# Kernel tuning notes

Measured on AMD Instinct MI355X. Metric: run time of the kernel, lower is better.

Reference implementation:

```python
import jax, jax.numpy as jnp
import numpy as np

B, T, V = 4, 2048, 2048
D = 256   # state_dim
R = 512   # inner_dim
EPS = float(jnp.finfo(jnp.float32).eps)  # F.rms_norm default eps = dtype eps


def rms_norm(x):
    return x * jax.lax.rsqrt(jnp.mean(x * x, axis=-1, keepdims=True) + EPS)


def setup_inputs() -> dict:
    key = jax.random.key(0)
    ks = jax.random.split(key, 9)
    std = 0.02
    return {
        "x": jax.random.normal(ks[0], (B, T, V), dtype=jnp.float32),
        "Wq": jax.random.normal(ks[1], (D, V), dtype=jnp.float32) * std,
        "Wk": jax.random.normal(ks[2], (D, V), dtype=jnp.float32) * std,
        "Wv": jax.random.normal(ks[3], (D, V), dtype=jnp.float32) * std,
        "Wo": jax.random.normal(ks[4], (V, D), dtype=jnp.float32) * std,
        "decay_logit": jnp.float32(3.0),
        "q_out_scale": jnp.float32(0.1),
        "Wdown": jax.random.normal(ks[5], (R, V), dtype=jnp.float32) * std,
        "Wup": jax.random.normal(ks[6], (V, R), dtype=jnp.float32) * std,
        "t_bias": jnp.zeros((R,), dtype=jnp.float32),
        "t_out_scale": jnp.float32(0.1),
        "q_scale": jnp.ones((1,), dtype=jnp.float32),
        "t_scale": jnp.ones((1,), dtype=jnp.float32),
    }


def qtable(x, Wq, Wk, Wv, Wo, decay_logit, out_scale):
    # x: (B,T,V)
    q = jnp.einsum('btv,dv->btd', x, Wq)
    k = jnp.einsum('btv,dv->btd', x, Wk)
    v = jnp.einsum('btv,dv->btd', x, Wv)
    scores = jnp.einsum('btd,bsd->bts', q, k)  # (B,T,T)
    decay = jax.nn.sigmoid(decay_logit)
    pos = jnp.arange(T)
    diff = pos[None, :] - pos[:, None]  # diff[t,s] = s - t ... matches torch (unsqueeze(0)-unsqueeze(1))
    causal = (diff > 0).astype(jnp.float32)
    weights = decay ** jnp.clip(diff.astype(jnp.float32) - 1.0, 0.0, None) * causal
    scores = scores * weights[None, :, :]
    retrieved = jnp.einsum('bts,bsd->btd', scores, v)
    return jnp.einsum('btd,vd->btv', retrieved, Wo) * out_scale


def transform(x, Wdown, Wup, bias, out_scale):
    h = jnp.einsum('btv,rv->btr', x, Wdown) + bias
    h = jax.nn.gelu(h, approximate=False)
    return jnp.einsum('btr,vr->btv', h, Wup) * out_scale


def reference(x, Wq, Wk, Wv, Wo, decay_logit, q_out_scale,
              Wdown, Wup, t_bias, t_out_scale, q_scale, t_scale):
    x = x + q_scale * qtable(rms_norm(x), Wq, Wk, Wv, Wo, decay_logit, q_out_scale)
    x = x + t_scale * transform(rms_norm(x), Wdown, Wup, t_bias, t_out_scale)
    return x
```

## Files before the change

kernel.cpp:

```cpp
#include <hip/hip_runtime.h>
#include <cmath>

typedef _Float16 f16;
typedef _Float16 f16x8 __attribute__((ext_vector_type(8)));
typedef _Float16 f16x4 __attribute__((ext_vector_type(4)));
typedef float f32x4 __attribute__((ext_vector_type(4)));

#define MFMA16(a, b, c) __builtin_amdgcn_mfma_f32_16x16x32_f16(a, b, c, 0, 0, 0)

static constexpr int Bsz = 4;
static constexpr int T = 2048;
static constexpr int V = 2048;
static constexpr int D = 256;
static constexpr int R = 512;
static constexpr int M = Bsz * T;

__device__ __forceinline__ void load_lds16(const f16* g, f16* l) {
    __builtin_amdgcn_global_load_lds(
        (const __attribute__((address_space(1))) unsigned int*)(unsigned long long)g,
        (__attribute__((address_space(3))) unsigned int*)(unsigned int)(unsigned long long)l,
        16, 0, 0);
}

__global__ __launch_bounds__(256) void conv_all(const float* __restrict__ s0,
                                                const float* __restrict__ s1,
                                                const float* __restrict__ s2,
                                                const float* __restrict__ s3,
                                                const float* __restrict__ s4,
                                                const float* __restrict__ s5,
                                                f16* __restrict__ dst) {
    int idx = (blockIdx.x * 256 + threadIdx.x) * 4;
    if (idx >= 4194304) return;
    const float* src; int off;
    if      (idx <  524288) { src = s0; off = idx; }
    else if (idx < 1048576) { src = s1; off = idx - 524288; }
    else if (idx < 1572864) { src = s2; off = idx - 1048576; }
    else if (idx < 2097152) { src = s3; off = idx - 1572864; }
    else if (idx < 3145728) { src = s4; off = idx - 2097152; }
    else                    { src = s5; off = idx - 3145728; }
    float4 v = *(const float4*)&src[off];
    f16x4 o;
    o[0] = (f16)v.x; o[1] = (f16)v.y; o[2] = (f16)v.z; o[3] = (f16)v.w;
    *(f16x4*)&dst[idx] = o;
}

__global__ __launch_bounds__(256) void rmsnorm_kernel(const float* __restrict__ x,
                                                      f16* __restrict__ out) {
    int row = blockIdx.x;
    const float* xr = x + (size_t)row * V;
    int tid = threadIdx.x;
    float4 v0 = ((const float4*)xr)[tid];
    float4 v1 = ((const float4*)xr)[tid + 256];
    float ss = v0.x * v0.x + v0.y * v0.y + v0.z * v0.z + v0.w * v0.w
             + v1.x * v1.x + v1.y * v1.y + v1.z * v1.z + v1.w * v1.w;
    #pragma unroll
    for (int o = 32; o > 0; o >>= 1) ss += __shfl_xor(ss, o);
    __shared__ float wsum[4];
    if ((tid & 63) == 0) wsum[tid >> 6] = ss;
    __syncthreads();
    float tot = wsum[0] + wsum[1] + wsum[2] + wsum[3];
    float s = rsqrtf(tot / (float)V + 1.1920929e-07f);
    f16* orow = out + (size_t)row * V;
    f16x4 o0, o1;
    o0[0] = (f16)(v0.x * s); o0[1] = (f16)(v0.y * s);
    o0[2] = (f16)(v0.z * s); o0[3] = (f16)(v0.w * s);
    o1[0] = (f16)(v1.x * s); o1[1] = (f16)(v1.y * s);
    o1[2] = (f16)(v1.z * s); o1[3] = (f16)(v1.w * s);
    *(f16x4*)&orow[tid * 4] = o0;
    *(f16x4*)&orow[1024 + tid * 4] = o1;
}

__global__ __launch_bounds__(256) void rmsnorm_f16(const f16* __restrict__ x,
                                                   f16* __restrict__ out) {
    int row = blockIdx.x;
    int tid = threadIdx.x;
    const f16* xr = x + (size_t)row * V;
    f16x8 v = *(const f16x8*)&xr[tid * 8];
    float f[8];
    float ss = 0.f;
    #pragma unroll
    for (int j = 0; j < 8; j++) { f[j] = (float)v[j]; ss += f[j] * f[j]; }
    #pragma unroll
    for (int o = 32; o > 0; o >>= 1) ss += __shfl_xor(ss, o);
    __shared__ float wsum[4];
    if ((tid & 63) == 0) wsum[tid >> 6] = ss;
    __syncthreads();
    float tot = wsum[0] + wsum[1] + wsum[2] + wsum[3];
    float s = rsqrtf(tot / (float)V + 1.1920929e-07f);
    f16x8 o;
    #pragma unroll
    for (int j = 0; j < 8; j++) o[j] = (f16)(f[j] * s);
    *(f16x8*)&out[(size_t)row * V + tid * 8] = o;
}

struct GemmEpi {
    const float* residf;
    const f16* residh;
    float* outf;
    f16* outh;
    f16* out_q; f16* out_k; f16* out_vT;
    f16* out_h;
    const float* bias;
    const float* sA; const float* sB;
};

template <int MODE>
__device__ __forceinline__ void epi_store(const GemmEpi& e, float s, f32x4 a,
                                          int gm_base, int gn) {
    #pragma unroll
    for (int i = 0; i < 4; i++) {
        int gm = gm_base + i;
        float vv = a[i];
        if (MODE == 0) {
            if (gn < 256) {
                e.out_q[(size_t)gm * D + gn] = (f16)vv;
            } else if (gn < 512) {
                e.out_k[(size_t)gm * D + (gn - 256)] = (f16)vv;
            } else {
                int d = gn - 512;
                int b = gm >> 11, t = gm & 2047;
                e.out_vT[((size_t)b * D + d) * T + t] = (f16)vv;
            }
        } else if (MODE == 1) {
            size_t o = (size_t)gm * V + gn;
            e.outh[o] = (f16)(e.residf[o] + s * vv);
        } else if (MODE == 2) {
            float z = vv + e.bias[gn];
            float g = 0.5f * z * (1.f + erff(z * 0.70710678118654752f));
            e.out_h[(size_t)gm * R + gn] = (f16)g;
        } else {
            size_t o = (size_t)gm * V + gn;
            e.outf[o] = (float)e.residh[o] + s * vv;
        }
    }
}

template <int MODE>
__global__ __launch_bounds__(256) void gemm_nt(const f16* __restrict__ A,
                                               const f16* __restrict__ Bm,
                                               int K, GemmEpi e) {
    __shared__ f16 Asl[2][128 * 32];
    __shared__ f16 Bsl[2][128 * 32];
    int tid = threadIdx.x;
    int lane = tid & 63, wv = tid >> 6;
    int wm = wv >> 1, wn = wv & 1;
    int quad = lane >> 4, l16 = lane & 15;
    int m0 = blockIdx.x * 128, n0 = blockIdx.y * 128;
    f32x4 acc[4][4] = {};

    int srow = lane >> 2;
    int scg = (lane & 3) ^ ((lane >> 3) & 3);
    const f16* Ag0 = &A[(size_t)(m0 + 16 * wv + srow) * K + scg * 8];
    const f16* Ag1 = &A[(size_t)(m0 + 16 * (wv + 4) + srow) * K + scg * 8];
    const f16* Bg0 = &Bm[(size_t)(n0 + 16 * wv + srow) * K + scg * 8];
    const f16* Bg1 = &Bm[(size_t)(n0 + 16 * (wv + 4) + srow) * K + scg * 8];
    int lo0 = (16 * wv) * 32, lo1 = (16 * (wv + 4)) * 32;

    int fs = quad ^ ((l16 >> 1) & 3);
    int niter = K >> 5;

    load_lds16(Ag0, &Asl[0][lo0]);
    load_lds16(Ag1, &Asl[0][lo1]);
    load_lds16(Bg0, &Bsl[0][lo0]);
    load_lds16(Bg1, &Bsl[0][lo1]);

    for (int i = 0; i < niter; i++) {
        int cur = i & 1;
        __builtin_amdgcn_s_barrier();
        if (i + 1 < niter) {
            int k0 = (i + 1) << 5;
            int nb = cur ^ 1;
            load_lds16(Ag0 + k0, &Asl[nb][lo0]);
            load_lds16(Ag1 + k0, &Asl[nb][lo1]);
            load_lds16(Bg0 + k0, &Bsl[nb][lo0]);
            load_lds16(Bg1 + k0, &Bsl[nb][lo1]);
            asm volatile("s_waitcnt vmcnt(4)" ::: "memory");
        } else {
            asm volatile("s_waitcnt vmcnt(0)" ::: "memory");
        }
        __builtin_amdgcn_s_barrier();
        f16x8 af[4], bf[4];
        #pragma unroll
        for (int j = 0; j < 4; j++)
            af[j] = *(const f16x8*)&Asl[cur][(64 * wm + 16 * j + l16) * 32 + fs * 8];
        #pragma unroll
        for (int j = 0; j < 4; j++)
            bf[j] = *(const f16x8*)&Bsl[cur][(64 * wn + 16 * j + l16) * 32 + fs * 8];
        #pragma unroll
        for (int mi = 0; mi < 4; mi++)
            #pragma unroll
            for (int ni = 0; ni < 4; ni++)
                acc[mi][ni] = MFMA16(af[mi], bf[ni], acc[mi][ni]);
    }

    float s = 0.f;
    if (MODE == 1 || MODE == 3) s = e.sA[0] * e.sB[0];
    #pragma unroll
    for (int mi = 0; mi < 4; mi++)
        #pragma unroll
        for (int ni = 0; ni < 4; ni++)
            epi_store<MODE>(e, s, acc[mi][ni],
                            m0 + 64 * wm + 16 * mi + quad * 4,
                            n0 + 64 * wn + 16 * ni + l16);
}

template <int MODE>
__global__ __launch_bounds__(512) void gemm_nt_sk(const f16* __restrict__ A,
                                                  const f16* __restrict__ Bm,
                                                  int K, GemmEpi e) {
    __shared__ f16 SL[2][2][2][128 * 32];
    int tid = threadIdx.x;
    int lane = tid & 63, wv = tid >> 6;
    int g = wv >> 2, wvg = wv & 3;
    int wm = wvg >> 1, wn = wvg & 1;
    int quad = lane >> 4, l16 = lane & 15;
    int m0 = blockIdx.x * 128, n0 = blockIdx.y * 128;
    f32x4 acc[4][4] = {};

    int Kg = K >> 1;
    int kbase = g * Kg;
    int srow = lane >> 2;
    int scg = (lane & 3) ^ ((lane >> 3) & 3);
    const f16* Ag0 = &A[(size_t)(m0 + 16 * wvg + srow) * K + kbase + scg * 8];
    const f16* Ag1 = &A[(size_t)(m0 + 16 * (wvg + 4) + srow) * K + kbase + scg * 8];
    const f16* Bg0 = &Bm[(size_t)(n0 + 16 * wvg + srow) * K + kbase + scg * 8];
    const f16* Bg1 = &Bm[(size_t)(n0 + 16 * (wvg + 4) + srow) * K + kbase + scg * 8];
    int lo0 = (16 * wvg) * 32, lo1 = (16 * (wvg + 4)) * 32;

    int fs = quad ^ ((l16 >> 1) & 3);
    int niter = Kg >> 5;

    load_lds16(Ag0, &SL[0][g][0][lo0]);
    load_lds16(Ag1, &SL[0][g][0][lo1]);
    load_lds16(Bg0, &SL[1][g][0][lo0]);
    load_lds16(Bg1, &SL[1][g][0][lo1]);

    for (int i = 0; i < niter; i++) {
        int cur = i & 1;
        __builtin_amdgcn_s_barrier();
        if (i + 1 < niter) {
            int k0 = (i + 1) << 5;
            int nb = cur ^ 1;
            load_lds16(Ag0 + k0, &SL[0][g][nb][lo0]);
            load_lds16(Ag1 + k0, &SL[0][g][nb][lo1]);
            load_lds16(Bg0 + k0, &SL[1][g][nb][lo0]);
            load_lds16(Bg1 + k0, &SL[1][g][nb][lo1]);
            asm volatile("s_waitcnt vmcnt(4)" ::: "memory");
        } else {
            asm volatile("s_waitcnt vmcnt(0)" ::: "memory");
        }
        __builtin_amdgcn_s_barrier();
        f16x8 af[4], bf[4];
        #pragma unroll
        for (int j = 0; j < 4; j++)
            af[j] = *(const f16x8*)&SL[0][g][cur][(64 * wm + 16 * j + l16) * 32 + fs * 8];
        #pragma unroll
        for (int j = 0; j < 4; j++)
            bf[j] = *(const f16x8*)&SL[1][g][cur][(64 * wn + 16 * j + l16) * 32 + fs * 8];
        #pragma unroll
        for (int mi = 0; mi < 4; mi++)
            #pragma unroll
            for (int ni = 0; ni < 4; ni++)
                acc[mi][ni] = MFMA16(af[mi], bf[ni], acc[mi][ni]);
    }

    __syncthreads();
    float* comb = (float*)&SL[0][0][0][0];
    {
        int mw = g ? 0 : 2;
        float* dst = comb + g * 8192 + wvg * 2048 + lane * 4;
        #pragma unroll
        for (int mm = 0; mm < 2; mm++)
            #pragma unroll
            for (int ni = 0; ni < 4; ni++)
                *(f32x4*)&dst[(mm * 4 + ni) * 256] = acc[mw + mm][ni];
    }
    __syncthreads();
    float s = 0.f;
    if (MODE == 1 || MODE == 3) s = e.sA[0] * e.sB[0];
    {
        int mf = g ? 2 : 0;
        const float* src = comb + (1 - g) * 8192 + wvg * 2048 + lane * 4;
        #pragma unroll
        for (int mm = 0; mm < 2; mm++) {
            #pragma unroll
            for (int ni = 0; ni < 4; ni++) {
                f32x4 a = acc[mf + mm][ni];
                a += *(const f32x4*)&src[(mm * 4 + ni) * 256];
                epi_store<MODE>(e, s, a,
                                m0 + 64 * wm + 16 * (mf + mm) + quad * 4,
                                n0 + 64 * wn + 16 * ni + l16);
            }
        }
    }
}

__global__ __launch_bounds__(256) void attn_kernel(const f16* __restrict__ q,
                                                   const f16* __restrict__ k,
                                                   const f16* __restrict__ vT,
                                                   f16* __restrict__ ret,
                                                   const float* __restrict__ decay_logit) {
    __shared__ f16 Psl[32 * 72];
    int tid = threadIdx.x, lane = tid & 63, wv = tid >> 6;
    int quad = lane >> 4, l16 = lane & 15;
    int b = blockIdx.y, t0 = blockIdx.x * 32;
    const f16* qb = q + (size_t)b * T * D;
    const f16* kb = k + (size_t)b * T * D;
    const f16* vb = vT + (size_t)b * D * T;
    f16* rb = ret + (size_t)b * T * D;

    float dl = decay_logit[0];
    float decay = 1.f / (1.f + expf(-dl));
    float l2d = log2f(decay);
    float nl2d = -l2d;

    f16x8 qf[2][8];
    #pragma unroll
    for (int mi = 0; mi < 2; mi++)
        #pragma unroll
        for (int kk = 0; kk < 8; kk++)
            qf[mi][kk] = *(const f16x8*)&qb[(size_t)(t0 + 16 * mi + l16) * D + kk * 32 + quad * 8];

    f32x4 acc2[2][4] = {};

    for (int s0 = t0; s0 < T; s0 += 64) {
        if ((float)(s0 - t0 - 32) * nl2d > 25.f) break;
        int srow = s0 + 16 * wv + l16;
        int srcl = srow < T ? srow : T - 1;
        f32x4 sacc[2] = {};
        #pragma unroll
        for (int kk = 0; kk < 8; kk++) {
            f16x8 bf = *(const f16x8*)&kb[(size_t)srcl * D + kk * 32 + quad * 8];
            sacc[0] = MFMA16(qf[0][kk], bf, sacc[0]);
            sacc[1] = MFMA16(qf[1][kk], bf, sacc[1]);
        }
        __syncthreads();
        #pragma unroll
        for (int mi = 0; mi < 2; mi++) {
            #pragma unroll
            for (int i = 0; i < 4; i++) {
                int t_ = t0 + 16 * mi + quad * 4 + i;
                int diff = srow - t_;
                float w = (diff > 0 && srow < T) ? exp2f((float)(diff - 1) * l2d) : 0.f;
                Psl[(16 * mi + quad * 4 + i) * 72 + 16 * wv + l16] = (f16)(sacc[mi][i] * w);
            }
        }
        __syncthreads();
        #pragma unroll
        for (int kk = 0; kk < 2; kk++) {
            int sb = s0 + kk * 32 + quad * 8;
            if (sb >= T) sb = T - 8;
            f16x8 pa[2], vf[4];
            #pragma unroll
            for (int mi = 0; mi < 2; mi++)
                pa[mi] = *(const f16x8*)&Psl[(16 * mi + l16) * 72 + kk * 32 + quad * 8];
            #pragma unroll
            for (int ni = 0; ni < 4; ni++)
                vf[ni] = *(const f16x8*)&vb[(size_t)(64 * wv + 16 * ni + l16) * T + sb];
            #pragma unroll
            for (int mi = 0; mi < 2; mi++)
                #pragma unroll
                for (int ni = 0; ni < 4; ni++)
                    acc2[mi][ni] = MFMA16(pa[mi], vf[ni], acc2[mi][ni]);
        }
    }

    #pragma unroll
    for (int mi = 0; mi < 2; mi++) {
        #pragma unroll
        for (int ni = 0; ni < 4; ni++) {
            int t_ = t0 + 16 * mi + quad * 4;
            int d_ = 64 * wv + 16 * ni + l16;
            #pragma unroll
            for (int i = 0; i < 4; i++)
                rb[(size_t)(t_ + i) * D + d_] = (f16)acc2[mi][ni][i];
        }
    }
}

extern "C" void kernel_launch(void* const* d_in, const int* in_sizes, int n_in,
                              void* d_out, int out_size, void* d_ws, size_t ws_size,
                              hipStream_t stream) {
    const float* x           = (const float*)d_in[0];
    const float* Wq          = (const float*)d_in[1];
    const float* Wk          = (const float*)d_in[2];
    const float* Wv          = (const float*)d_in[3];
    const float* Wo          = (const float*)d_in[4];
    const float* decay_logit = (const float*)d_in[5];
    const float* q_out_scale = (const float*)d_in[6];
    const float* Wdown       = (const float*)d_in[7];
    const float* Wup         = (const float*)d_in[8];
    const float* t_bias      = (const float*)d_in[9];
    const float* t_out_scale = (const float*)d_in[10];
    const float* q_scale     = (const float*)d_in[11];
    const float* t_scale     = (const float*)d_in[12];

    char* ws = (char*)d_ws;
    f16* Wqkv16  = (f16*)ws;  ws += (size_t)768 * V * 2;
    f16* Wo16    = (f16*)ws;  ws += (size_t)V * D * 2;
    f16* Wdown16 = (f16*)ws;  ws += (size_t)R * V * 2;
    f16* Wup16   = (f16*)ws;  ws += (size_t)V * R * 2;
    f16* xn16    = (f16*)ws;  ws += (size_t)M * V * 2;
    f16* q16     = (f16*)ws;  ws += (size_t)M * D * 2;
    f16* k16     = (f16*)ws;  ws += (size_t)M * D * 2;
    f16* vT16    = (f16*)ws;  ws += (size_t)Bsz * D * T * 2;
    f16* ret16   = (f16*)ws;  ws += (size_t)M * D * 2;
    f16* x2_16   = (f16*)ws;  ws += (size_t)M * V * 2;
    f16* h16     = q16;

    float* out = (float*)d_out;

    conv_all<<<dim3(4096), 256, 0, stream>>>(Wq, Wk, Wv, Wo, Wdown, Wup, Wqkv16);

    rmsnorm_kernel<<<dim3(M), 256, 0, stream>>>(x, xn16);

    {
        GemmEpi e = {};
        e.out_q = q16; e.out_k = k16; e.out_vT = vT16;
        gemm_nt_sk<0><<<dim3(M / 128, 768 / 128), 512, 0, stream>>>(xn16, Wqkv16, V, e);
    }

    attn_kernel<<<dim3(T / 32, Bsz), 256, 0, stream>>>(q16, k16, vT16, ret16, decay_logit);

    {
        GemmEpi e = {};
        e.residf = x; e.outh = x2_16; e.sA = q_scale; e.sB = q_out_scale;
        gemm_nt<1><<<dim3(M / 128, V / 128), 256, 0, stream>>>(ret16, Wo16, D, e);
    }

    rmsnorm_f16<<<dim3(M), 256, 0, stream>>>(x2_16, xn16);

    {
        GemmEpi e = {};
        e.out_h = h16; e.bias = t_bias;
        gemm_nt_sk<2><<<dim3(M / 128, R / 128), 512, 0, stream>>>(xn16, Wdown16, V, e);
    }

    {
        GemmEpi e = {};
        e.residh = x2_16; e.outf = out; e.sA = t_scale; e.sB = t_out_scale;
        gemm_nt<3><<<dim3(M / 128, V / 128), 256, 0, stream>>>(h16, Wup16, R, e);
    }
}
```

Before: 359.8 us.

## Replace split-K 512-thread GEMM with 256-thread K=64 tile GEMM

```diff
diff --git a/kernel.cpp b/kernel.cpp
--- a/kernel.cpp
+++ b/kernel.cpp
@@ -205,94 +205,84 @@
 }
 
 template <int MODE>
-__global__ __launch_bounds__(512) void gemm_nt_sk(const f16* __restrict__ A,
-                                                  const f16* __restrict__ Bm,
-                                                  int K, GemmEpi e) {
-    __shared__ f16 SL[2][2][2][128 * 32];
+__global__ __launch_bounds__(256) void gemm_nt_k64(const f16* __restrict__ A,
+                                                   const f16* __restrict__ Bm,
+                                                   int K, GemmEpi e) {
+    __shared__ f16 Asl[2][128 * 64];
+    __shared__ f16 Bsl[2][128 * 64];
     int tid = threadIdx.x;
     int lane = tid & 63, wv = tid >> 6;
-    int g = wv >> 2, wvg = wv & 3;
-    int wm = wvg >> 1, wn = wvg & 1;
+    int wm = wv >> 1, wn = wv & 1;
     int quad = lane >> 4, l16 = lane & 15;
     int m0 = blockIdx.x * 128, n0 = blockIdx.y * 128;
     f32x4 acc[4][4] = {};
 
-    int Kg = K >> 1;
-    int kbase = g * Kg;
-    int srow = lane >> 2;
-    int scg = (lane & 3) ^ ((lane >> 3) & 3);
-    const f16* Ag0 = &A[(size_t)(m0 + 16 * wvg + srow) * K + kbase + scg * 8];
-    const f16* Ag1 = &A[(size_t)(m0 + 16 * (wvg + 4) + srow) * K + kbase + scg * 8];
-    const f16* Bg0 = &Bm[(size_t)(n0 + 16 * wvg + srow) * K + kbase + scg * 8];
-    const f16* Bg1 = &Bm[(size_t)(n0 + 16 * (wvg + 4) + srow) * K + kbase + scg * 8];
-    int lo0 = (16 * wvg) * 32, lo1 = (16 * (wvg + 4)) * 32;
-
-    int fs = quad ^ ((l16 >> 1) & 3);
-    int niter = Kg >> 5;
-
-    load_lds16(Ag0, &SL[0][g][0][lo0]);
-    load_lds16(Ag1, &SL[0][g][0][lo1]);
-    load_lds16(Bg0, &SL[1][g][0][lo0]);
-    load_lds16(Bg1, &SL[1][g][0][lo1]);
+    int r8 = lane >> 3;
+    int gcol = (lane & 7) ^ r8;
+    const f16* Ag[4]; const f16* Bg[4]; int lo[4];
+    #pragma unroll
+    for (int j = 0; j < 4; j++) {
+        int rbase = 8 * (wv + 4 * j);
+        Ag[j] = &A[(size_t)(m0 + rbase + r8) * K + gcol * 8];
+        Bg[j] = &Bm[(size_t)(n0 + rbase + r8) * K + gcol * 8];
+        lo[j] = rbase * 64;
+    }
+    int niter = K >> 6;
+
+    #pragma unroll
+    for (int j = 0; j < 4; j++) {
+        load_lds16(Ag[j], &Asl[0][lo[j]]);
+        load_lds16(Bg[j], &Bsl[0][lo[j]]);
+    }
 
     for (int i = 0; i < niter; i++) {
         int cur = i & 1;
         __builtin_amdgcn_s_barrier();
         if (i + 1 < niter) {
-            int k0 = (i + 1) << 5;
+            int k0 = (i + 1) << 6;
             int nb = cur ^ 1;
-            load_lds16(Ag0 + k0, &SL[0][g][nb][lo0]);
-            load_lds16(Ag1 + k0, &SL[0][g][nb][lo1]);
-            load_lds16(Bg0 + k0, &SL[1][g][nb][lo0]);
-            load_lds16(Bg1 + k0, &SL[1][g][nb][lo1]);
-            asm volatile("s_waitcnt vmcnt(4)" ::: "memory");
+            #pragma unroll
+            for (int j = 0; j < 4; j++) {
+                load_lds16(Ag[j] + k0, &Asl[nb][lo[j]]);
+                load_lds16(Bg[j] + k0, &Bsl[nb][lo[j]]);
+            }
+            asm volatile("s_waitcnt vmcnt(8)" ::: "memory");
         } else {
             asm volatile("s_waitcnt vmcnt(0)" ::: "memory");
         }
         __builtin_amdgcn_s_barrier();
-        f16x8 af[4], bf[4];
-        #pragma unroll
-        for (int j = 0; j < 4; j++)
-            af[j] = *(const f16x8*)&SL[0][g][cur][(64 * wm + 16 * j + l16) * 32 + fs * 8];
-        #pragma unroll
-        for (int j = 0; j < 4; j++)
-            bf[j] = *(const f16x8*)&SL[1][g][cur][(64 * wn + 16 * j + l16) * 32 + fs * 8];
-        #pragma unroll
-        for (int mi = 0; mi < 4; mi++)
-            #pragma unroll
-            for (int ni = 0; ni < 4; ni++)
-                acc[mi][ni] = MFMA16(af[mi], bf[ni], acc[mi][ni]);
-    }
-
-    __syncthreads();
-    float* comb = (float*)&SL[0][0][0][0];
-    {
-        int mw = g ? 0 : 2;
-        float* dst = comb + g * 8192 + wvg * 2048 + lane * 4;
-        #pragma unroll
-        for (int mm = 0; mm < 2; mm++)
-            #pragma unroll
-            for (int ni = 0; ni < 4; ni++)
-                *(f32x4*)&dst[(mm * 4 + ni) * 256] = acc[mw + mm][ni];
-    }
-    __syncthreads();
+        #pragma unroll
+        for (int kk = 0; kk < 2; kk++) {
+            f16x8 af[4], bf[4];
+            #pragma unroll
+            for (int j = 0; j < 4; j++) {
+                int row = 64 * wm + 16 * j + l16;
+                int sl = (kk * 4 + quad) ^ (l16 & 7);
+                af[j] = *(const f16x8*)&Asl[cur][row * 64 + sl * 8];
+            }
+            #pragma unroll
+            for (int j = 0; j < 4; j++) {
+                int row = 64 * wn + 16 * j + l16;
+                int sl = (kk * 4 + quad) ^ (l16 & 7);
+                bf[j] = *(const f16x8*)&Bsl[cur][row * 64 + sl * 8];
+            }
+            #pragma unroll
+            for (int mi = 0; mi < 4; mi++)
+                #pragma unroll
+                for (int ni = 0; ni < 4; ni++)
+                    acc[mi][ni] = MFMA16(af[mi], bf[ni], acc[mi][ni]);
+        }
+    }
+
     float s = 0.f;
     if (MODE == 1 || MODE == 3) s = e.sA[0] * e.sB[0];
-    {
-        int mf = g ? 2 : 0;
-        const float* src = comb + (1 - g) * 8192 + wvg * 2048 + lane * 4;
-        #pragma unroll
-        for (int mm = 0; mm < 2; mm++) {
-            #pragma unroll
-            for (int ni = 0; ni < 4; ni++) {
-                f32x4 a = acc[mf + mm][ni];
-                a += *(const f32x4*)&src[(mm * 4 + ni) * 256];
-                epi_store<MODE>(e, s, a,
-                                m0 + 64 * wm + 16 * (mf + mm) + quad * 4,
-                                n0 + 64 * wn + 16 * ni + l16);
-            }
-        }
-    }
+    #pragma unroll
+    for (int mi = 0; mi < 4; mi++)
+        #pragma unroll
+        for (int ni = 0; ni < 4; ni++)
+            epi_store<MODE>(e, s, acc[mi][ni],
+                            m0 + 64 * wm + 16 * mi + quad * 4,
+                            n0 + 64 * wn + 16 * ni + l16);
 }
 
 __global__ __launch_bounds__(256) void attn_kernel(const f16* __restrict__ q,
@@ -417,7 +407,7 @@
     {
         GemmEpi e = {};
         e.out_q = q16; e.out_k = k16; e.out_vT = vT16;
-        gemm_nt_sk<0><<<dim3(M / 128, 768 / 128), 512, 0, stream>>>(xn16, Wqkv16, V, e);
+        gemm_nt_k64<0><<<dim3(M / 128, 768 / 128), 256, 0, stream>>>(xn16, Wqkv16, V, e);
     }
 
     attn_kernel<<<dim3(T / 32, Bsz), 256, 0, stream>>>(q16, k16, vT16, ret16, decay_logit);
@@ -433,7 +423,7 @@
     {
         GemmEpi e = {};
         e.out_h = h16; e.bias = t_bias;
-        gemm_nt_sk<2><<<dim3(M / 128, R / 128), 512, 0, stream>>>(xn16, Wdown16, V, e);
+        gemm_nt_k64<2><<<dim3(M / 128, R / 128), 256, 0, stream>>>(xn16, Wdown16, V, e);
     }
 
     {
```

New measurement: 318.6 us. 11.5% less time.
